# Kernel optimization log

Hardware: AMD Instinct MI355X
Metric: run time of the kernel (lower is better)

## Reference

```python
import jax, jax.numpy as jnp
import numpy as np

B, D, LD, LP = 8, 192, 128, 1024
FC = [1024, 1024, 512]
NC = 2


def setup_inputs() -> dict:
    key = jax.random.key(0)
    ks = jax.random.split(key, 18)
    s = 0.05  # small init scale for numerical sanity
    inp = {
        "drug_conv": jax.random.normal(ks[0], (B, D, LD), jnp.float32),
        "protein_conv": jax.random.normal(ks[1], (B, D, LP), jnp.float32),
        "Wd": jax.random.normal(ks[2], (D, D), jnp.float32) * s,
        "bd": jax.random.normal(ks[3], (D,), jnp.float32) * s,
        "Wp": jax.random.normal(ks[4], (D, D), jnp.float32) * s,
        "bp": jax.random.normal(ks[5], (D,), jnp.float32) * s,
        "Wa": jax.random.normal(ks[6], (D, D), jnp.float32) * s,
        "ba": jax.random.normal(ks[7], (D,), jnp.float32) * s,
        "W1": jax.random.normal(ks[8], (FC[0], 2 * D), jnp.float32) * s,
        "b1": jax.random.normal(ks[9], (FC[0],), jnp.float32) * s,
        "W2": jax.random.normal(ks[10], (FC[1], FC[0]), jnp.float32) * s,
        "b2": jax.random.normal(ks[11], (FC[1],), jnp.float32) * s,
        "W3": jax.random.normal(ks[12], (FC[2], FC[1]), jnp.float32) * s,
        "b3": jax.random.normal(ks[13], (FC[2],), jnp.float32) * s,
        "Wo": jax.random.normal(ks[14], (NC, FC[2]), jnp.float32) * s,
        "bo": jax.random.normal(ks[15], (NC,), jnp.float32) * s,
    }
    return inp


def reference(drug_conv, protein_conv, Wd, bd, Wp, bp, Wa, ba,
              W1, b1, W2, b2, W3, b3, Wo, bo):
    # drug_conv: (B, D, Ld); protein_conv: (B, D, Lp). Torch Linear: y = x @ W.T + b
    d_att = jnp.einsum('bdl,ed->ble', drug_conv, Wd) + bd      # (B, Ld, D)
    p_att = jnp.einsum('bdl,ed->ble', protein_conv, Wp) + bp   # (B, Lp, D)
    # broadcast additive cross-attention: (B, Ld, Lp, D)
    h = jax.nn.relu(d_att[:, :, None, :] + p_att[:, None, :, :])
    A = jnp.einsum('blpd,ed->blpe', h, Wa) + ba                # (B, Ld, Lp, D)
    comp_att = jax.nn.sigmoid(jnp.mean(A, axis=2))             # (B, Ld, D)
    prot_att = jax.nn.sigmoid(jnp.mean(A, axis=1))             # (B, Lp, D)
    # gated residual: x*0.5 + x*att  (att permuted back to (B, D, L))
    drug = drug_conv * (0.5 + jnp.transpose(comp_att, (0, 2, 1)))
    prot = protein_conv * (0.5 + jnp.transpose(prot_att, (0, 2, 1)))
    # MaxPool1d over full sequence length == max along last axis
    drug_pooled = jnp.max(drug, axis=2)                        # (B, D)
    prot_pooled = jnp.max(prot, axis=2)                        # (B, D)
    pair = jnp.concatenate([drug_pooled, prot_pooled], axis=1) # (B, 2D)
    lrelu = lambda x: jax.nn.leaky_relu(x, 0.01)
    h1 = lrelu(pair @ W1.T + b1)
    h2 = lrelu(h1 @ W2.T + b2)
    h3 = lrelu(h2 @ W3.T + b3)
    return h3 @ Wo.T + bo                                      # (B, num_classes)
```

## Files before the change

### kernel.cpp

```cpp
#include <hip/hip_runtime.h>
#include <math.h>

#define BB 8
#define DD 192
#define LLD 128
#define LLP 1024
#define FC1 1024
#define FC2 1024
#define FC3 512
#define NCLS 2
#define LT 8

__global__ void proj_both_kernel(const float* __restrict__ drug,
                                 const float* __restrict__ prot,
                                 const float* __restrict__ Wd,
                                 const float* __restrict__ bdv,
                                 const float* __restrict__ Wp,
                                 const float* __restrict__ bpv,
                                 float* __restrict__ d_att,
                                 float* __restrict__ p_att) {
    int blk = blockIdx.x;
    const float *x, *W, *bias;
    float* y;
    int L, b, l0;
    if (blk < BB * (LLD / LT)) {
        x = drug; W = Wd; bias = bdv; y = d_att; L = LLD;
        b = blk >> 4; l0 = (blk & 15) * LT;
    } else {
        int idx = blk - BB * (LLD / LT);
        x = prot; W = Wp; bias = bpv; y = p_att; L = LLP;
        b = idx >> 7; l0 = (idx & 127) * LT;
    }
    int tid = threadIdx.x;

    __shared__ float xs[LT][DD + 4];

    const float* xbase = x + (size_t)b * DD * L + l0;
#pragma unroll
    for (int k = 0; k < LT; ++k) {
        int idx = tid + k * DD;
        int d = idx >> 3;
        int j = idx & (LT - 1);
        xs[j][d] = xbase[(size_t)d * L + j];
    }
    __syncthreads();

    const int e = tid;
    const float be = bias[e];
    float acc[LT];
#pragma unroll
    for (int j = 0; j < LT; ++j) acc[j] = be;

    const float4* Wr4 = (const float4*)(W + (size_t)e * DD);
#pragma unroll 2
    for (int d4 = 0; d4 < DD / 4; ++d4) {
        float4 w = Wr4[d4];
#pragma unroll
        for (int j = 0; j < LT; ++j) {
            float4 h = *(const float4*)&xs[j][d4 * 4];
            acc[j] = fmaf(h.x, w.x, acc[j]);
            acc[j] = fmaf(h.y, w.y, acc[j]);
            acc[j] = fmaf(h.z, w.z, acc[j]);
            acc[j] = fmaf(h.w, w.w, acc[j]);
        }
    }

    float* ybase = y + ((size_t)b * L + l0) * DD;
#pragma unroll
    for (int j = 0; j < LT; ++j)
        ybase[(size_t)j * DD + e] = acc[j];
}

__global__ void cross_sort_kernel(const float* __restrict__ da,
                                  const float* __restrict__ pa,
                                  float* __restrict__ Hd_t,
                                  float* __restrict__ Hp_t) {
    int blk = blockIdx.x;
    int b = blk / (DD / 2);
    int dp = blk - b * (DD / 2);
    int d0 = dp * 2;
    int tid = threadIdx.x;

    __shared__ float skey[2][LLD];
    __shared__ int   sidx[2][LLD];
    __shared__ float sufs[2][LLD + 1];
    __shared__ int   cnt[2][LLD + 1];
    __shared__ float val[2][LLD + 1];

    {
        int a = tid >> 7, l = tid & 127;
        skey[a][l] = da[((size_t)b * LLD + l) * DD + d0 + a];
        sidx[a][l] = l;
    }
    for (int i = tid; i < 2 * (LLD + 1); i += 256) {
        int a = i / (LLD + 1), k = i - a * (LLD + 1);
        cnt[a][k] = 0;
        val[a][k] = 0.f;
    }
    if (tid < 2) sufs[tid][LLD] = 0.f;
    __syncthreads();

    {
        int a = tid >> 7, i = tid & 127;
        for (int k = 2; k <= LLD; k <<= 1) {
            for (int j = k >> 1; j > 0; j >>= 1) {
                int ixj = i ^ j;
                if (ixj > i) {
                    float ki = skey[a][i], kj = skey[a][ixj];
                    bool up = ((i & k) == 0);
                    if ((ki > kj) == up) {
                        skey[a][i] = kj; skey[a][ixj] = ki;
                        int t = sidx[a][i]; sidx[a][i] = sidx[a][ixj]; sidx[a][ixj] = t;
                    }
                }
                __syncthreads();
            }
        }
    }

    {
        int a = tid >> 7, i = tid & 127;
        sufs[a][i] = skey[a][i];
        __syncthreads();
        for (int off = 1; off < LLD; off <<= 1) {
            float v = (i + off < LLD) ? sufs[a][i + off] : 0.f;
            __syncthreads();
            sufs[a][i] += v;
            __syncthreads();
        }
    }

    {
        int d_i = tid & 1, prow = tid >> 1;
        float* hprow = Hp_t + ((size_t)b * DD + d0 + d_i) * LLP;
        const float* qbase = pa + (size_t)b * LLP * DD + d0 + d_i;
#pragma unroll
        for (int batch = 0; batch < LLP / 128; ++batch) {
            int p = batch * 128 + prow;
            float q = qbase[(size_t)p * DD];
            float nq = -q;
            int pos = 0;
#pragma unroll
            for (int st = LLD; st > 0; st >>= 1) {
                int np = pos + st;
                if (np <= LLD && skey[d_i][np - 1] <= nq) pos = np;
            }
            hprow[p] = ((float)(LLD - pos) * q + sufs[d_i][pos]) * (1.0f / LLD);
            atomicAdd(&cnt[d_i][pos], 1);
            atomicAdd(&val[d_i][pos], q);
        }
    }
    __syncthreads();

    {
        int a = tid >> 7, i = tid & 127;
        for (int off = 1; off < LLD; off <<= 1) {
            int c = 0; float v = 0.f;
            if (i >= off) { c = cnt[a][i - off]; v = val[a][i - off]; }
            __syncthreads();
            cnt[a][i] += c;
            val[a][i] += v;
            __syncthreads();
        }
    }

    {
        int a = tid >> 7, r = tid & 127;
        float hv = (skey[a][r] * (float)cnt[a][r] + val[a][r]) * (1.0f / LLP);
        Hd_t[((size_t)b * DD + d0 + a) * LLD + sidx[a][r]] = hv;
    }
}

__global__ void gemm_sig_both_kernel(const float* __restrict__ Hd_t,
                                     const float* __restrict__ Hp_t,
                                     const float* __restrict__ Wa,
                                     const float* __restrict__ ba,
                                     float* __restrict__ catt_t,
                                     float* __restrict__ psig_t) {
    int blk = blockIdx.x;
    const float* Ht;
    float* out_t;
    int L, b, l0;
    if (blk < BB * (LLD / LT)) {
        b = blk >> 4; l0 = (blk & 15) * LT;
        Ht = Hd_t; out_t = catt_t; L = LLD;
    } else {
        int idx = blk - BB * (LLD / LT);
        b = idx >> 7; l0 = (idx & 127) * LT;
        Ht = Hp_t; out_t = psig_t; L = LLP;
    }
    int tid = threadIdx.x;

    __shared__ float hs[LT][DD + 4];
    __shared__ float cs[LT][DD + 1];

    const float* hrow = Ht + ((size_t)b * DD + tid) * L + l0;
#pragma unroll
    for (int j = 0; j < LT; ++j) hs[j][tid] = hrow[j];
    __syncthreads();

    const int e = tid;
    const float bias = ba[e];
    float acc[LT];
#pragma unroll
    for (int j = 0; j < LT; ++j) acc[j] = bias;

    const float4* Wr4 = (const float4*)(Wa + (size_t)e * DD);
#pragma unroll 2
    for (int d4 = 0; d4 < DD / 4; ++d4) {
        float4 w = Wr4[d4];
#pragma unroll
        for (int j = 0; j < LT; ++j) {
            float4 h = *(const float4*)&hs[j][d4 * 4];
            acc[j] = fmaf(h.x, w.x, acc[j]);
            acc[j] = fmaf(h.y, w.y, acc[j]);
            acc[j] = fmaf(h.z, w.z, acc[j]);
            acc[j] = fmaf(h.w, w.w, acc[j]);
        }
    }

#pragma unroll
    for (int j = 0; j < LT; ++j)
        cs[j][e] = 1.0f / (1.0f + __expf(-acc[j]));
    __syncthreads();

    float* obase = out_t + (size_t)b * DD * L + l0;
    for (int k = tid; k < LT * DD; k += DD) {
        int eo = k >> 3;
        int j = k & (LT - 1);
        obase[(size_t)eo * L + j] = cs[j][eo];
    }
}

__global__ void pool_pair_kernel(const float* __restrict__ drug,
                                 const float* __restrict__ prot,
                                 const float* __restrict__ catt_t,
                                 const float* __restrict__ psig_t,
                                 float* __restrict__ pair) {
    int bd = blockIdx.x;
    int b = bd / DD;
    int d = bd - b * DD;
    int lane = threadIdx.x;

    const float* dr = drug + (size_t)bd * LLD;
    const float* ca = catt_t + (size_t)bd * LLD;
    float m1 = -INFINITY;
#pragma unroll
    for (int k = 0; k < LLD / 64; ++k) {
        int l = lane + 64 * k;
        m1 = fmaxf(m1, dr[l] * (0.5f + ca[l]));
    }

    const float* pr = prot + (size_t)bd * LLP;
    const float* ps = psig_t + (size_t)bd * LLP;
    float m2 = -INFINITY;
#pragma unroll
    for (int k = 0; k < LLP / 64; ++k) {
        int p = lane + 64 * k;
        m2 = fmaxf(m2, pr[p] * (0.5f + ps[p]));
    }

#pragma unroll
    for (int off = 32; off > 0; off >>= 1) {
        m1 = fmaxf(m1, __shfl_xor(m1, off));
        m2 = fmaxf(m2, __shfl_xor(m2, off));
    }
    if (lane == 0) {
        pair[b * 2 * DD + d] = m1;
        pair[b * 2 * DD + DD + d] = m2;
    }
}

__global__ void fc_wave_kernel(const float* __restrict__ x,
                               const float* __restrict__ W,
                               const float* __restrict__ bias,
                               float* __restrict__ y,
                               int K, int N, int leaky) {
    int gtid = blockIdx.x * blockDim.x + threadIdx.x;
    int wid = gtid >> 6;
    int lane = gtid & 63;
    if (wid >= BB * N) return;
    int b = wid / N;
    int j = wid - b * N;
    const float4* xr = (const float4*)(x + (size_t)b * K);
    const float4* Wr = (const float4*)(W + (size_t)j * K);
    int K4 = K >> 2;
    float s = 0.f;
    for (int k = lane; k < K4; k += 64) {
        float4 xv = xr[k];
        float4 wv = Wr[k];
        s = fmaf(xv.x, wv.x, s);
        s = fmaf(xv.y, wv.y, s);
        s = fmaf(xv.z, wv.z, s);
        s = fmaf(xv.w, wv.w, s);
    }
#pragma unroll
    for (int off = 32; off > 0; off >>= 1) s += __shfl_xor(s, off);
    if (lane == 0) {
        float acc = s + bias[j];
        if (leaky) acc = (acc > 0.f) ? acc : 0.01f * acc;
        y[wid] = acc;
    }
}

extern "C" void kernel_launch(void* const* d_in, const int* in_sizes, int n_in,
                              void* d_out, int out_size, void* d_ws, size_t ws_size,
                              hipStream_t stream) {
    const float* drug = (const float*)d_in[0];
    const float* prot = (const float*)d_in[1];
    const float* Wd = (const float*)d_in[2];
    const float* bd = (const float*)d_in[3];
    const float* Wp = (const float*)d_in[4];
    const float* bp = (const float*)d_in[5];
    const float* Wa = (const float*)d_in[6];
    const float* ba = (const float*)d_in[7];
    const float* W1 = (const float*)d_in[8];
    const float* b1 = (const float*)d_in[9];
    const float* W2 = (const float*)d_in[10];
    const float* b2 = (const float*)d_in[11];
    const float* W3 = (const float*)d_in[12];
    const float* b3 = (const float*)d_in[13];
    const float* Wo = (const float*)d_in[14];
    const float* bo = (const float*)d_in[15];
    float* out = (float*)d_out;

    float* ws = (float*)d_ws;
    const size_t n_datt = (size_t)BB * LLD * DD;
    const size_t n_patt = (size_t)BB * LLP * DD;
    float* d_att  = ws;
    float* p_att  = d_att + n_datt;
    float* Hd_t   = p_att + n_patt;
    float* Hp_t   = Hd_t + n_datt;
    float* catt_t = Hp_t + n_patt;
    float* psig_t = catt_t + n_datt;
    float* pair   = psig_t + n_patt;
    float* h1     = pair + (size_t)BB * 2 * DD;
    float* h2     = h1 + (size_t)BB * FC1;
    float* h3     = h2 + (size_t)BB * FC2;

    proj_both_kernel<<<BB * (LLD / LT) + BB * (LLP / LT), DD, 0, stream>>>(
        drug, prot, Wd, bd, Wp, bp, d_att, p_att);

    cross_sort_kernel<<<BB * (DD / 2), 256, 0, stream>>>(d_att, p_att, Hd_t, Hp_t);

    gemm_sig_both_kernel<<<BB * (LLD / LT) + BB * (LLP / LT), DD, 0, stream>>>(
        Hd_t, Hp_t, Wa, ba, catt_t, psig_t);

    pool_pair_kernel<<<BB * DD, 64, 0, stream>>>(drug, prot, catt_t, psig_t, pair);

    fc_wave_kernel<<<(BB * FC1 * 64) / 256, 256, 0, stream>>>(pair, W1, b1, h1, 2 * DD, FC1, 1);
    fc_wave_kernel<<<(BB * FC2 * 64) / 256, 256, 0, stream>>>(h1, W2, b2, h2, FC1, FC2, 1);
    fc_wave_kernel<<<(BB * FC3 * 64) / 256, 256, 0, stream>>>(h2, W3, b3, h3, FC2, FC3, 1);
    fc_wave_kernel<<<(BB * NCLS * 64 + 255) / 256, 256, 0, stream>>>(h3, Wo, bo, out, FC3, NCLS, 0);
}
```

Measured before the change: 99.49 us.

## Fuse sigmoid gating and max-pool into attention GEMM via atomic float max

The separate pooling kernel is removed. The attention GEMM now applies the sigmoid gate to the input tile and reduces a partial max per output channel, which it merges into the pair buffer with an integer-based atomic float max. The pair buffer is initialised to -inf inside the earlier sort kernel. This drops one kernel launch and the write and re-read of the full gate tensors, at the cost of many global atomics on a small buffer and a dependency on the initialisation order across kernels.

```diff
diff --git a/kernel.cpp b/kernel.cpp
--- a/kernel.cpp
+++ b/kernel.cpp
@@ -10,6 +10,13 @@
 #define FC3 512
 #define NCLS 2
 #define LT 8
+
+__device__ __forceinline__ void atomicMaxFloat(float* addr, float value) {
+    if (value >= 0.f)
+        atomicMax((int*)addr, __float_as_int(value));
+    else
+        atomicMin((unsigned int*)addr, __float_as_uint(value));
+}
 
 __global__ void proj_both_kernel(const float* __restrict__ drug,
                                  const float* __restrict__ prot,
@@ -74,7 +81,8 @@
 __global__ void cross_sort_kernel(const float* __restrict__ da,
                                   const float* __restrict__ pa,
                                   float* __restrict__ Hd_t,
-                                  float* __restrict__ Hp_t) {
+                                  float* __restrict__ Hp_t,
+                                  float* __restrict__ pair) {
     int blk = blockIdx.x;
     int b = blk / (DD / 2);
     int dp = blk - b * (DD / 2);
@@ -86,6 +94,12 @@
     __shared__ float sufs[2][LLD + 1];
     __shared__ int   cnt[2][LLD + 1];
     __shared__ float val[2][LLD + 1];
+
+    if (tid < 4) {
+        int side = tid >> 1;
+        int dd = d0 + (tid & 1);
+        pair[b * 2 * DD + side * DD + dd] = -INFINITY;
+    }
 
     {
         int a = tid >> 7, l = tid & 127;
@@ -171,28 +185,28 @@
     }
 }
 
-__global__ void gemm_sig_both_kernel(const float* __restrict__ Hd_t,
+__global__ void gemm_sig_pool_kernel(const float* __restrict__ Hd_t,
                                      const float* __restrict__ Hp_t,
                                      const float* __restrict__ Wa,
                                      const float* __restrict__ ba,
-                                     float* __restrict__ catt_t,
-                                     float* __restrict__ psig_t) {
+                                     const float* __restrict__ drug,
+                                     const float* __restrict__ prot,
+                                     float* __restrict__ pair) {
     int blk = blockIdx.x;
     const float* Ht;
-    float* out_t;
-    int L, b, l0;
+    const float* xsrc;
+    int L, b, l0, side;
     if (blk < BB * (LLD / LT)) {
         b = blk >> 4; l0 = (blk & 15) * LT;
-        Ht = Hd_t; out_t = catt_t; L = LLD;
+        Ht = Hd_t; xsrc = drug; L = LLD; side = 0;
     } else {
         int idx = blk - BB * (LLD / LT);
         b = idx >> 7; l0 = (idx & 127) * LT;
-        Ht = Hp_t; out_t = psig_t; L = LLP;
+        Ht = Hp_t; xsrc = prot; L = LLP; side = 1;
     }
     int tid = threadIdx.x;
 
     __shared__ float hs[LT][DD + 4];
-    __shared__ float cs[LT][DD + 1];
 
     const float* hrow = Ht + ((size_t)b * DD + tid) * L + l0;
 #pragma unroll
@@ -219,56 +233,17 @@
         }
     }
 
-#pragma unroll
-    for (int j = 0; j < LT; ++j)
-        cs[j][e] = 1.0f / (1.0f + __expf(-acc[j]));
-    __syncthreads();
-
-    float* obase = out_t + (size_t)b * DD * L + l0;
-    for (int k = tid; k < LT * DD; k += DD) {
-        int eo = k >> 3;
-        int j = k & (LT - 1);
-        obase[(size_t)eo * L + j] = cs[j][eo];
-    }
-}
-
-__global__ void pool_pair_kernel(const float* __restrict__ drug,
-                                 const float* __restrict__ prot,
-                                 const float* __restrict__ catt_t,
-                                 const float* __restrict__ psig_t,
-                                 float* __restrict__ pair) {
-    int bd = blockIdx.x;
-    int b = bd / DD;
-    int d = bd - b * DD;
-    int lane = threadIdx.x;
-
-    const float* dr = drug + (size_t)bd * LLD;
-    const float* ca = catt_t + (size_t)bd * LLD;
-    float m1 = -INFINITY;
-#pragma unroll
-    for (int k = 0; k < LLD / 64; ++k) {
-        int l = lane + 64 * k;
-        m1 = fmaxf(m1, dr[l] * (0.5f + ca[l]));
-    }
-
-    const float* pr = prot + (size_t)bd * LLP;
-    const float* ps = psig_t + (size_t)bd * LLP;
-    float m2 = -INFINITY;
-#pragma unroll
-    for (int k = 0; k < LLP / 64; ++k) {
-        int p = lane + 64 * k;
-        m2 = fmaxf(m2, pr[p] * (0.5f + ps[p]));
-    }
-
-#pragma unroll
-    for (int off = 32; off > 0; off >>= 1) {
-        m1 = fmaxf(m1, __shfl_xor(m1, off));
-        m2 = fmaxf(m2, __shfl_xor(m2, off));
-    }
-    if (lane == 0) {
-        pair[b * 2 * DD + d] = m1;
-        pair[b * 2 * DD + DD + d] = m2;
-    }
+    const float* xrow = xsrc + ((size_t)b * DD + e) * L + l0;
+    float4 x0 = *(const float4*)&xrow[0];
+    float4 x1 = *(const float4*)&xrow[4];
+    float xv[LT] = {x0.x, x0.y, x0.z, x0.w, x1.x, x1.y, x1.z, x1.w};
+    float m = -INFINITY;
+#pragma unroll
+    for (int j = 0; j < LT; ++j) {
+        float gate = 0.5f + 1.0f / (1.0f + __expf(-acc[j]));
+        m = fmaxf(m, xv[j] * gate);
+    }
+    atomicMaxFloat(&pair[b * 2 * DD + side * DD + e], m);
 }
 
 __global__ void fc_wave_kernel(const float* __restrict__ x,
@@ -331,9 +306,7 @@
     float* p_att  = d_att + n_datt;
     float* Hd_t   = p_att + n_patt;
     float* Hp_t   = Hd_t + n_datt;
-    float* catt_t = Hp_t + n_patt;
-    float* psig_t = catt_t + n_datt;
-    float* pair   = psig_t + n_patt;
+    float* pair   = Hp_t + n_patt;
     float* h1     = pair + (size_t)BB * 2 * DD;
     float* h2     = h1 + (size_t)BB * FC1;
     float* h3     = h2 + (size_t)BB * FC2;
@@ -341,12 +314,10 @@
     proj_both_kernel<<<BB * (LLD / LT) + BB * (LLP / LT), DD, 0, stream>>>(
         drug, prot, Wd, bd, Wp, bp, d_att, p_att);
 
-    cross_sort_kernel<<<BB * (DD / 2), 256, 0, stream>>>(d_att, p_att, Hd_t, Hp_t);
-
-    gemm_sig_both_kernel<<<BB * (LLD / LT) + BB * (LLP / LT), DD, 0, stream>>>(
-        Hd_t, Hp_t, Wa, ba, catt_t, psig_t);
-
-    pool_pair_kernel<<<BB * DD, 64, 0, stream>>>(drug, prot, catt_t, psig_t, pair);
+    cross_sort_kernel<<<BB * (DD / 2), 256, 0, stream>>>(d_att, p_att, Hd_t, Hp_t, pair);
+
+    gemm_sig_pool_kernel<<<BB * (LLD / LT) + BB * (LLP / LT), DD, 0, stream>>>(
+        Hd_t, Hp_t, Wa, ba, drug, prot, pair);
 
     fc_wave_kernel<<<(BB * FC1 * 64) / 256, 256, 0, stream>>>(pair, W1, b1, h1, 2 * DD, FC1, 1);
     fc_wave_kernel<<<(BB * FC2 * 64) / 256, 256, 0, stream>>>(h1, W2, b2, h2, FC1, FC2, 1);
```

Measured after the change: 94.50 us, median of 2. 5.0% less time.
